# Kernel tuning notes

Hardware: AMD Instinct MI355X
Metric: run time of the kernel (lower is better)

## Reference

```python
import jax, jax.numpy as jnp
jax.config.update("jax_enable_x64", True)  # morton codes need int64 bit tricks
import numpy as np

B = 8
N_POINTS = 131072
PATCH = 32
STRIDE = 16
RES = 1024
D_MODEL = 256
L = (N_POINTS - PATCH) // STRIDE + 1  # 8191


def setup_inputs() -> dict:
    key = jax.random.key(0)
    ks = jax.random.split(key, 11)
    def lin_w(k, fin, fout):
        return (jax.random.normal(k, (fin, fout), jnp.float32) / np.sqrt(fin)).astype(jnp.float32)
    return {
        "points": jax.random.normal(ks[0], (B, N_POINTS, 3), jnp.float32),
        # LocalGeometryEncoder mlp: 3 -> 64 -> 128 (ReLU after both)
        "W1": lin_w(ks[1], 3, 64), "b1": jnp.zeros((64,), jnp.float32),
        "W2": lin_w(ks[2], 64, 128), "b2": jnp.zeros((128,), jnp.float32),
        # PositionalEncoding mlp: 3 -> 64 -> 128 (ReLU only after first)
        "Wp1": lin_w(ks[3], 3, 64), "bp1": jnp.zeros((64,), jnp.float32),
        "Wp2": lin_w(ks[4], 64, 128), "bp2": jnp.zeros((128,), jnp.float32),
        # projection: 256 -> d_model
        "Wproj": lin_w(ks[5], 256, D_MODEL), "bproj": jnp.zeros((D_MODEL,), jnp.float32),
    }


def _expand_bits(v):
    v = v.astype(jnp.int64)
    v = (v | (v << 32)) & jnp.int64(8725724278095871)
    v = (v | (v << 16)) & jnp.int64(8725728556220671)
    v = (v | (v << 8)) & jnp.int64(1157144660301377551)
    v = (v | (v << 4)) & jnp.int64(1207822528635744451)
    v = (v | (v << 2)) & jnp.int64(1317624576693539401)
    return v


def _morton_code(points):
    p_min = points.min(axis=1, keepdims=True)
    p_max = points.max(axis=1, keepdims=True)
    scale = jnp.clip(p_max - p_min, 1e-8, None)
    normed = (points - p_min) / scale
    q = jnp.clip((normed * (RES - 1)).astype(jnp.int64), 0, RES - 1)  # [B,N,3]
    return _expand_bits(q[..., 0]) * 4 + _expand_bits(q[..., 1]) * 2 + _expand_bits(q[..., 2])


def reference(points, W1, b1, W2, b2, Wp1, bp1, Wp2, bp2, Wproj, bproj):
    # z-order sort
    morton = _morton_code(points)                 # [B,N] int64
    sort_idx = jnp.argsort(morton, axis=1)        # [B,N]
    sp = jnp.take_along_axis(points, sort_idx[..., None], axis=1)  # [B,N,3]
    # sliding-window unfold -> [B,L,P,3]
    win = jnp.arange(L)[:, None] * STRIDE + jnp.arange(PATCH)[None, :]  # [L,P]
    patches = sp[:, win, :]
    # local geometry encoder
    centroids = patches.mean(axis=2)              # [B,L,3]
    local = patches - centroids[:, :, None, :]    # [B,L,P,3]
    h = jax.nn.relu(jnp.einsum('blpc,cd->blpd', local, W1) + b1)
    feat = jax.nn.relu(jnp.einsum('blpd,de->blpe', h, W2) + b2)  # [B,L,P,128]
    geo = feat.max(axis=2)                        # [B,L,128]
    # positional encoding of centroids
    pos = jax.nn.relu(centroids @ Wp1 + bp1) @ Wp2 + bp2  # [B,L,128]
    combined = jnp.concatenate([geo, pos], axis=-1)       # [B,L,256]
    tokens = combined @ Wproj + bproj                     # [B,L,d_model]
    return tokens, centroids, sort_idx
```

## Files before the change

kernel.cpp:

```cpp
#include <hip/hip_runtime.h>
#include <hip/hip_bf16.h>
#include <stdint.h>

#define B_SZ   8
#define N_PTS  131072
#define L_TOK  8191
#define M_TOK  (B_SZ * L_TOK)

typedef unsigned long long u64;
typedef unsigned int u32;
typedef unsigned short u16;
typedef __hip_bfloat16 bf16;
typedef float f32x4 __attribute__((ext_vector_type(4)));
typedef short bf16x8 __attribute__((ext_vector_type(8)));
typedef u32 u32x4 __attribute__((ext_vector_type(4)));

__device__ __forceinline__ u16 f2bf(float f) {
  u32 u = __float_as_uint(f);
  u32 r = u + 0x7FFFu + ((u >> 16) & 1u);
  return (u16)(r >> 16);
}
__device__ __forceinline__ float bf2f(u16 s) {
  return __uint_as_float(((u32)s) << 16);
}

__device__ __forceinline__ void split_pair(float h0, float h1, u32& hp, u32& lp) {
  asm("v_cvt_pk_bf16_f32 %0, %1, %2" : "=v"(hp) : "v"(h0), "v"(h1));
  float r0 = __uint_as_float(hp << 16);
  float r1 = __uint_as_float(hp & 0xFFFF0000u);
  asm("v_cvt_pk_bf16_f32 %0, %1, %2" : "=v"(lp) : "v"(h0 - r0), "v"(h1 - r1));
}
__device__ __forceinline__ bf16x8 asbf(u32x4 x) {
  union { u32x4 a; bf16x8 b; } u; u.a = x; return u.b;
}

__device__ __forceinline__ u32 f2u_mono(float f) {
  u32 u = __float_as_uint(f);
  return (u & 0x80000000u) ? ~u : (u | 0x80000000u);
}
__device__ __forceinline__ float u2f_mono(u32 u) {
  u32 b = (u & 0x80000000u) ? (u ^ 0x80000000u) : ~u;
  return __uint_as_float(b);
}

__global__ void init_mm_kernel(u32* mm) {
  int t = threadIdx.x;
  if (t < 48) mm[t] = ((t % 6) < 3) ? 0xFFFFFFFFu : 0u;
}

__global__ __launch_bounds__(256) void minmax_kernel(const float* __restrict__ pts,
                                                     u32* __restrict__ mm) {
  int b = blockIdx.x >> 6;
  int chunk = blockIdx.x & 63;
  int base = b * N_PTS + chunk * 2048;
  float mn0 = 3.4e38f, mn1 = 3.4e38f, mn2 = 3.4e38f;
  float mx0 = -3.4e38f, mx1 = -3.4e38f, mx2 = -3.4e38f;
  for (int i = threadIdx.x; i < 2048; i += 256) {
    const float* p = pts + (size_t)(base + i) * 3;
    float x = p[0], y = p[1], z = p[2];
    mn0 = fminf(mn0, x); mx0 = fmaxf(mx0, x);
    mn1 = fminf(mn1, y); mx1 = fmaxf(mx1, y);
    mn2 = fminf(mn2, z); mx2 = fmaxf(mx2, z);
  }
  __shared__ u32 smn[3], smx[3];
  if (threadIdx.x < 3) { smn[threadIdx.x] = 0xFFFFFFFFu; smx[threadIdx.x] = 0u; }
  __syncthreads();
  atomicMin(&smn[0], f2u_mono(mn0)); atomicMin(&smn[1], f2u_mono(mn1)); atomicMin(&smn[2], f2u_mono(mn2));
  atomicMax(&smx[0], f2u_mono(mx0)); atomicMax(&smx[1], f2u_mono(mx1)); atomicMax(&smx[2], f2u_mono(mx2));
  __syncthreads();
  if (threadIdx.x < 3)       atomicMin(&mm[b * 6 + threadIdx.x], smn[threadIdx.x]);
  else if (threadIdx.x < 6)  atomicMax(&mm[b * 6 + threadIdx.x], smx[threadIdx.x - 3]);
}

__device__ __forceinline__ u64 expand_bits(u64 v) {
  v = (v | (v << 32)) & 0x001F00000000FFFFull;
  v = (v | (v << 16)) & 0x001F0000FF0000FFull;
  v = (v | (v << 8))  & 0x100F00F00F00F00Full;
  v = (v | (v << 4))  & 0x10C30C30C30C30C3ull;
  v = (v | (v << 2))  & 0x1249249249249249ull;
  return v;
}

__device__ __forceinline__ long long quant1(float p, float mn, float mx) {
  float scale = fmaxf(mx - mn, 1e-8f);
  float num = p - mn;
  float rcp = 1.0f / scale;
  asm volatile("" : "+v"(rcp));
  float normed = num * rcp;
  asm volatile("" : "+v"(normed));
  float scaled = normed * 1023.0f;
  asm volatile("" : "+v"(scaled));
  long long q = (long long)scaled;
  q = q < 0 ? 0 : q; q = q > 1023 ? 1023 : q;
  return q;
}

__global__ __launch_bounds__(256) void morton_kernel(const float* __restrict__ pts,
                                                     const u32* __restrict__ mm,
                                                     u64* __restrict__ keys) {
  int gid = blockIdx.x * 256 + threadIdx.x;
  int b = gid >> 17;
  int i = gid & (N_PTS - 1);
  const u32* mb = mm + b * 6;
  float mn0 = u2f_mono(mb[0]), mn1 = u2f_mono(mb[1]), mn2 = u2f_mono(mb[2]);
  float mx0 = u2f_mono(mb[3]), mx1 = u2f_mono(mb[4]), mx2 = u2f_mono(mb[5]);
  const float* p = pts + (size_t)gid * 3;
  long long q0 = quant1(p[0], mn0, mx0);
  long long q1 = quant1(p[1], mn1, mx1);
  long long q2 = quant1(p[2], mn2, mx2);
  u64 m = expand_bits((u64)q0) * 4ull + expand_bits((u64)q1) * 2ull + expand_bits((u64)q2);
  keys[gid] = (m << 17) | (u64)i;
}

__global__ __launch_bounds__(256) void radix_hist(const u64* __restrict__ keys,
                                                  u32* __restrict__ hist, int shift) {
  int blk = blockIdx.x;
  int b = blk >> 8, c = blk & 255;
  int t = threadIdx.x;
  __shared__ u32 h[256];
  h[t] = 0;
  __syncthreads();
  size_t base = ((size_t)b << 17) + (size_t)c * 512;
  u32 d0 = (u32)((keys[base + t] >> shift) & 255ull);
  u32 d1 = (u32)((keys[base + 256 + t] >> shift) & 255ull);
  atomicAdd(&h[d0], 1u);
  atomicAdd(&h[d1], 1u);
  __syncthreads();
  hist[(blk << 8) + t] = h[t];
}

__global__ __launch_bounds__(256) void radix_scan_a(u32* __restrict__ hist,
                                                    u32* __restrict__ tot) {
  int blk = blockIdx.x;
  int b = blk >> 3, dg = blk & 7;
  int t = threadIdx.x;
  __shared__ u32 H[32 * 257];
  __shared__ u32 part[32 * 8];
  for (int i = t; i < 8192; i += 256) {
    int c = i >> 5, d5 = i & 31;
    H[d5 * 257 + c] = hist[((b * 256 + c) << 8) + dg * 32 + d5];
  }
  __syncthreads();
  int d5 = t & 31, sub = t >> 5;
  u32 s = 0;
  for (int c = sub * 32; c < sub * 32 + 32; ++c) s += H[d5 * 257 + c];
  part[d5 * 8 + sub] = s;
  __syncthreads();
  u32 run = 0;
  for (int k = 0; k < sub; ++k) run += part[d5 * 8 + k];
  if (sub == 7) tot[(b << 8) + dg * 32 + d5] = run + s;
  for (int c = sub * 32; c < sub * 32 + 32; ++c) {
    u32 x = H[d5 * 257 + c];
    H[d5 * 257 + c] = run;
    run += x;
  }
  __syncthreads();
  for (int i = t; i < 8192; i += 256) {
    int c = i >> 5, d5b = i & 31;
    hist[((b * 256 + c) << 8) + dg * 32 + d5b] = H[d5b * 257 + c];
  }
}

__global__ __launch_bounds__(256) void radix_scan_b(const u32* __restrict__ tot,
                                                    u32* __restrict__ dbase) {
  int b = blockIdx.x;
  int t = threadIdx.x;
  __shared__ u32 s[256];
  u32 my = tot[(b << 8) + t];
  s[t] = my;
  __syncthreads();
  for (int off = 1; off < 256; off <<= 1) {
    u32 v = (t >= off) ? s[t - off] : 0u;
    __syncthreads();
    s[t] += v;
    __syncthreads();
  }
  dbase[(b << 8) + t] = s[t] - my;
}

__global__ __launch_bounds__(512) void radix_scatter(const u64* __restrict__ keys_in,
                                                     u64* __restrict__ keys_out,
                                                     const u32* __restrict__ hist,
                                                     const u32* __restrict__ dbase,
                                                     int shift) {
  int blk = blockIdx.x;
  int b = blk >> 8, c = blk & 255;
  int t = threadIdx.x;
  int w = t >> 6, lane = t & 63;
  __shared__ u32 whist[8][256];
  __shared__ u32 gbase[256];
  for (int i = t; i < 2048; i += 512) ((u32*)whist)[i] = 0u;
  if (t < 256) gbase[t] = hist[(blk << 8) + t] + dbase[(b << 8) + t];
  __syncthreads();
  size_t base = ((size_t)b << 17) + (size_t)c * 512;
  u64 key = keys_in[base + t];
  u32 d = (u32)((key >> shift) & 255ull);
  u64 m = ~0ull;
  #pragma unroll
  for (int k = 0; k < 8; ++k) {
    u64 bb = __ballot((d >> k) & 1u);
    m &= ((d >> k) & 1u) ? bb : ~bb;
  }
  u32 rank = (u32)__popcll(m & ((1ull << lane) - 1ull));
  int leader = (int)(__ffsll((unsigned long long)m)) - 1;
  if (lane == (u32)leader) whist[w][d] = (u32)__popcll(m);
  __syncthreads();
  if (t < 256) {
    u32 run = 0;
    #pragma unroll
    for (int ww = 0; ww < 8; ++ww) { u32 v = whist[ww][t]; whist[ww][t] = run; run += v; }
  }
  __syncthreads();
  u32 dst = gbase[d] + whist[w][d] + rank;
  keys_out[((size_t)b << 17) + dst] = key;
}

__global__ __launch_bounds__(256) void extract_frag_kernel(
    const u64* __restrict__ keys, const float* __restrict__ pts,
    float* __restrict__ sp, float* __restrict__ sidx,
    const float* __restrict__ Wproj, const float* __restrict__ W2,
    const float* __restrict__ Wp2,
    u16* __restrict__ wfrag, u16* __restrict__ w2f, u16* __restrict__ wp2f) {
  int bid = blockIdx.x;
  int t = threadIdx.x;
  if (bid < 4096) {
    int gid = bid * 256 + t;
    u64 key = keys[gid];
    int idx = (int)(key & 0x1FFFFull);
    sidx[gid] = (float)idx;
    int b = gid >> 17;
    const float* src = pts + ((size_t)(b << 17) + idx) * 3;
    float* dst = sp + (size_t)gid * 3;
    dst[0] = src[0]; dst[1] = src[1]; dst[2] = src[2];
  } else {
    int fb = bid - 4096;
    if (fb < 256) {
      int e = fb * 256 + t;
      int k = e >> 8, n = e & 255;
      float v = Wproj[e];
      u16 hb = f2bf(v);
      u16 lb = f2bf(v - bf2f(hb));
      int ks = k >> 5, q = (k >> 3) & 3, j = k & 7;
      int nt = n >> 4, ln2 = n & 15;
      int base = ((ks * 16 + nt) * 64 + q * 16 + ln2) * 8 + j;
      wfrag[base] = hb;
      wfrag[65536 + base] = lb;
    } else {
      const float* W = (fb < 288) ? W2 : Wp2;
      u16* frag = (fb < 288) ? w2f : wp2f;
      int e = ((fb < 288) ? (fb - 256) : (fb - 288)) * 256 + t;
      int k = e >> 7, n = e & 127;
      float v = W[e];
      u16 hb = f2bf(v);
      u16 lb = f2bf(v - bf2f(hb));
      int kc = k >> 5, q = (k >> 3) & 3, j = k & 7;
      int nt = n >> 4, ln2 = n & 15;
      int base = ((kc * 8 + nt) * 64 + q * 16 + ln2) * 8 + j;
      frag[base] = hb;
      frag[8192 + base] = lb;
    }
  }
}

__global__ __launch_bounds__(512) void patch_kernel(
    const float* __restrict__ sp,
    const float* __restrict__ W1, const float* __restrict__ b1,
    const u16* __restrict__ W2g, const float* __restrict__ b2,
    const float* __restrict__ Wp1, const float* __restrict__ bp1,
    const u16* __restrict__ Wp2g, const float* __restrict__ bp2,
    bf16* __restrict__ comb, float* __restrict__ cent_out) {
  __shared__ float ptsS[6192];
  __shared__ float cenS[384];
  __shared__ float w1p[256];
  __shared__ float wpp[256];
  __shared__ float b2s[128];
  __shared__ float bp2s[128];
  __shared__ __align__(16) u16 W2frag[16384];

  int t = threadIdx.x;
  int bib = blockIdx.x;
  int b = blockIdx.y;
  int l0 = bib * 128;
  int pcount = min(128, L_TOK - l0);

  {
    const float4* src4 = (const float4*)(sp + (size_t)b * (N_PTS * 3) + (size_t)l0 * 48);
    int nvec = min(1548, ((N_PTS - l0 * 16) * 3) >> 2);
    float4* dst4 = (float4*)ptsS;
    for (int i = t; i < nvec; i += 512) dst4[i] = src4[i];
  }
  {
    const float4* s4 = (const float4*)W2g;
    float4* d4 = (float4*)W2frag;
    for (int i = t; i < 2048; i += 512) d4[i] = s4[i];
  }
  if (t < 64) {
    w1p[t] = W1[t]; w1p[64 + t] = W1[64 + t];
    w1p[128 + t] = W1[128 + t]; w1p[192 + t] = b1[t];
  } else if (t < 128) {
    int i = t - 64;
    wpp[i] = Wp1[i]; wpp[64 + i] = Wp1[64 + i];
    wpp[128 + i] = Wp1[128 + i]; wpp[192 + i] = bp1[i];
  } else if (t < 256) {
    b2s[t - 128] = b2[t - 128];
  } else if (t < 384) {
    bp2s[t - 256] = bp2[t - 256];
  }
  __syncthreads();

  if (t < 384) {
    int pa = t / 3, c = t - pa * 3;
    if (pa < pcount) {
      float s = 0.f;
      for (int i = 0; i < 32; ++i) {
        int ii = (i + pa) & 31;
        s += ptsS[(pa * 16 + ii) * 3 + c];
      }
      float cv = s * (1.0f / 32.0f);
      cenS[pa * 3 + c] = cv;
      cent_out[(size_t)(b * L_TOK + l0 + pa) * 3 + c] = cv;
    }
  }
  __syncthreads();

  int w = t >> 6, lane = t & 63, ln = lane & 15, quad = lane >> 4;
  const bf16x8* Bf = (const bf16x8*)W2frag;

  for (int ig = 0; ig < 16; ++ig) {
    int ll = w * 16 + ig;
    if (ll >= pcount) break;
    float cx = cenS[ll * 3], cy = cenS[ll * 3 + 1], cz = cenS[ll * 3 + 2];
    float xs[2], ys[2], zs[2];
    #pragma unroll
    for (int mt = 0; mt < 2; ++mt) {
      int row = ll * 16 + mt * 16 + ln;
      xs[mt] = ptsS[row * 3] - cx;
      ys[mt] = ptsS[row * 3 + 1] - cy;
      zs[mt] = ptsS[row * 3 + 2] - cz;
    }
    u32x4 Ahi[2][2], Alo[2][2];
    #pragma unroll
    for (int kc = 0; kc < 2; ++kc)
      #pragma unroll
      for (int w4 = 0; w4 < 4; ++w4) {
        int col = kc * 32 + quad * 8 + w4 * 2;
        float wx0 = w1p[col],     wy0 = w1p[64 + col],     wz0 = w1p[128 + col],     wb0 = w1p[192 + col];
        float wx1 = w1p[col + 1], wy1 = w1p[64 + col + 1], wz1 = w1p[128 + col + 1], wb1 = w1p[192 + col + 1];
        #pragma unroll
        for (int mt = 0; mt < 2; ++mt) {
          float h0 = fmaxf(fmaf(xs[mt], wx0, fmaf(ys[mt], wy0, fmaf(zs[mt], wz0, wb0))), 0.f);
          float h1 = fmaxf(fmaf(xs[mt], wx1, fmaf(ys[mt], wy1, fmaf(zs[mt], wz1, wb1))), 0.f);
          u32 hp, lp;
          split_pair(h0, h1, hp, lp);
          Ahi[mt][kc][w4] = hp;
          Alo[mt][kc][w4] = lp;
        }
      }
    bf16x8 Ah[2][2], Al[2][2];
    #pragma unroll
    for (int mt = 0; mt < 2; ++mt)
      #pragma unroll
      for (int kc = 0; kc < 2; ++kc) { Ah[mt][kc] = asbf(Ahi[mt][kc]); Al[mt][kc] = asbf(Alo[mt][kc]); }

    size_t tokoff = (size_t)(b * L_TOK + l0 + ll) * 256;
    #pragma unroll
    for (int half = 0; half < 2; ++half) {
      f32x4 acc[2][4];
      #pragma unroll
      for (int mt = 0; mt < 2; ++mt)
        #pragma unroll
        for (int n4 = 0; n4 < 4; ++n4) acc[mt][n4] = (f32x4){0.f, 0.f, 0.f, 0.f};
      #pragma unroll
      for (int n4 = 0; n4 < 4; ++n4) {
        int nt = half * 4 + n4;
        bf16x8 Bh0 = Bf[(0 * 8 + nt) * 64 + lane];
        bf16x8 Bh1 = Bf[(1 * 8 + nt) * 64 + lane];
        bf16x8 Bl0 = Bf[1024 + (0 * 8 + nt) * 64 + lane];
        bf16x8 Bl1 = Bf[1024 + (1 * 8 + nt) * 64 + lane];
        #pragma unroll
        for (int mt = 0; mt < 2; ++mt) {
          acc[mt][n4] = __builtin_amdgcn_mfma_f32_16x16x32_bf16(Ah[mt][0], Bh0, acc[mt][n4], 0, 0, 0);
          acc[mt][n4] = __builtin_amdgcn_mfma_f32_16x16x32_bf16(Ah[mt][1], Bh1, acc[mt][n4], 0, 0, 0);
          acc[mt][n4] = __builtin_amdgcn_mfma_f32_16x16x32_bf16(Al[mt][0], Bh0, acc[mt][n4], 0, 0, 0);
          acc[mt][n4] = __builtin_amdgcn_mfma_f32_16x16x32_bf16(Al[mt][1], Bh1, acc[mt][n4], 0, 0, 0);
          acc[mt][n4] = __builtin_amdgcn_mfma_f32_16x16x32_bf16(Ah[mt][0], Bl0, acc[mt][n4], 0, 0, 0);
          acc[mt][n4] = __builtin_amdgcn_mfma_f32_16x16x32_bf16(Ah[mt][1], Bl1, acc[mt][n4], 0, 0, 0);
        }
      }
      #pragma unroll
      for (int n4 = 0; n4 < 4; ++n4) {
        int col = (half * 4 + n4) * 16 + ln;
        float bv = b2s[col];
        float m = 0.f;
        #pragma unroll
        for (int mt = 0; mt < 2; ++mt)
          #pragma unroll
          for (int r = 0; r < 4; ++r) m = fmaxf(m, acc[mt][n4][r] + bv);
        m = fmaxf(m, __shfl_xor(m, 16));
        m = fmaxf(m, __shfl_xor(m, 32));
        if (lane < 16) comb[tokoff + col] = __float2bfloat16(m);
      }
    }
  }

  {
    int lrow = w * 16 + ln;
    int lcl = min(lrow, pcount - 1);
    float cx = cenS[lcl * 3], cy = cenS[lcl * 3 + 1], cz = cenS[lcl * 3 + 2];
    u32x4 Ahi[2], Alo[2];
    #pragma unroll
    for (int kc = 0; kc < 2; ++kc)
      #pragma unroll
      for (int w4 = 0; w4 < 4; ++w4) {
        int col = kc * 32 + quad * 8 + w4 * 2;
        float h0 = fmaxf(fmaf(cx, wpp[col], fmaf(cy, wpp[64 + col], fmaf(cz, wpp[128 + col], wpp[192 + col]))), 0.f);
        float h1 = fmaxf(fmaf(cx, wpp[col + 1], fmaf(cy, wpp[64 + col + 1], fmaf(cz, wpp[128 + col + 1], wpp[192 + col + 1]))), 0.f);
        u32 hp, lp;
        split_pair(h0, h1, hp, lp);
        Ahi[kc][w4] = hp;
        Alo[kc][w4] = lp;
      }
    bf16x8 A0h = asbf(Ahi[0]), A1h = asbf(Ahi[1]), A0l = asbf(Alo[0]), A1l = asbf(Alo[1]);
    const bf16x8* Pf = (const bf16x8*)Wp2g;
    f32x4 acc[8];
    #pragma unroll
    for (int nt = 0; nt < 8; ++nt) acc[nt] = (f32x4){0.f, 0.f, 0.f, 0.f};
    #pragma unroll
    for (int nt = 0; nt < 8; ++nt) {
      bf16x8 Bh0 = Pf[(0 * 8 + nt) * 64 + lane];
      bf16x8 Bh1 = Pf[(8 + nt) * 64 + lane];
      bf16x8 Bl0 = Pf[1024 + (0 * 8 + nt) * 64 + lane];
      bf16x8 Bl1 = Pf[1024 + (8 + nt) * 64 + lane];
      acc[nt] = __builtin_amdgcn_mfma_f32_16x16x32_bf16(A0h, Bh0, acc[nt], 0, 0, 0);
      acc[nt] = __builtin_amdgcn_mfma_f32_16x16x32_bf16(A1h, Bh1, acc[nt], 0, 0, 0);
      acc[nt] = __builtin_amdgcn_mfma_f32_16x16x32_bf16(A0l, Bh0, acc[nt], 0, 0, 0);
      acc[nt] = __builtin_amdgcn_mfma_f32_16x16x32_bf16(A1l, Bh1, acc[nt], 0, 0, 0);
      acc[nt] = __builtin_amdgcn_mfma_f32_16x16x32_bf16(A0h, Bl0, acc[nt], 0, 0, 0);
      acc[nt] = __builtin_amdgcn_mfma_f32_16x16x32_bf16(A1h, Bl1, acc[nt], 0, 0, 0);
    }
    #pragma unroll
    for (int nt = 0; nt < 8; ++nt)
      #pragma unroll
      for (int r = 0; r < 4; ++r) {
        int lr = w * 16 + quad * 4 + r;
        if (lr < pcount) {
          float v = acc[nt][r] + bp2s[nt * 16 + ln];
          comb[(size_t)(b * L_TOK + l0 + lr) * 256 + 128 + nt * 16 + ln] = __float2bfloat16(v);
        }
      }
  }
}

__global__ __launch_bounds__(256) void proj_mfma(const bf16* __restrict__ A,
                                                 const u16* __restrict__ fragG,
                                                 const float* __restrict__ bias,
                                                 float* __restrict__ C) {
  int t = threadIdx.x;
  int w = t >> 6, lane = t & 63, ln = lane & 15, quad = lane >> 4;
  int tile0 = blockIdx.x * 8 + w * 2;
  const bf16x8* Bf = (const bf16x8*)fragG;

  bf16x8 Af[2][8];
  const bf16x8 zero8 = (bf16x8){0, 0, 0, 0, 0, 0, 0, 0};
  #pragma unroll
  for (int mt = 0; mt < 2; ++mt) {
    int row = (tile0 + mt) * 16 + ln;
    bool ok = row < M_TOK;
    const bf16x8* ap = (const bf16x8*)(A + (size_t)(ok ? row : 0) * 256);
    #pragma unroll
    for (int ks = 0; ks < 8; ++ks) {
      bf16x8 v = ap[ks * 4 + quad];
      Af[mt][ks] = ok ? v : zero8;
    }
  }

  for (int nt = 0; nt < 16; ++nt) {
    f32x4 acc[2];
    #pragma unroll
    for (int mt = 0; mt < 2; ++mt) acc[mt] = (f32x4){0.f, 0.f, 0.f, 0.f};
    #pragma unroll
    for (int ks = 0; ks < 8; ++ks) {
      bf16x8 Bh = Bf[(ks * 16 + nt) * 64 + lane];
      bf16x8 Bl = Bf[8192 + (ks * 16 + nt) * 64 + lane];
      #pragma unroll
      for (int mt = 0; mt < 2; ++mt)
        acc[mt] = __builtin_amdgcn_mfma_f32_16x16x32_bf16(Af[mt][ks], Bh, acc[mt], 0, 0, 0);
      #pragma unroll
      for (int mt = 0; mt < 2; ++mt)
        acc[mt] = __builtin_amdgcn_mfma_f32_16x16x32_bf16(Af[mt][ks], Bl, acc[mt], 0, 0, 0);
    }
    int col = nt * 16 + ln;
    float bv = bias[col];
    #pragma unroll
    for (int mt = 0; mt < 2; ++mt)
      #pragma unroll
      for (int r = 0; r < 4; ++r) {
        int row = (tile0 + mt) * 16 + quad * 4 + r;
        if (row < M_TOK) C[(size_t)row * 256 + col] = acc[mt][r] + bv;
      }
  }
}

extern "C" void kernel_launch(void* const* d_in, const int* in_sizes, int n_in,
                              void* d_out, int out_size, void* d_ws, size_t ws_size,
                              hipStream_t stream) {
  const float* points = (const float*)d_in[0];
  const float* W1 = (const float*)d_in[1];
  const float* b1 = (const float*)d_in[2];
  const float* W2 = (const float*)d_in[3];
  const float* b2 = (const float*)d_in[4];
  const float* Wp1 = (const float*)d_in[5];
  const float* bp1 = (const float*)d_in[6];
  const float* Wp2 = (const float*)d_in[7];
  const float* bp2 = (const float*)d_in[8];
  const float* Wproj = (const float*)d_in[9];
  const float* bproj = (const float*)d_in[10];

  float* out = (float*)d_out;
  float* tokens = out;
  float* cents  = out + 16775168;
  float* sidx   = out + 16971752;

  char* ws = (char*)d_ws;
  u32* mm     = (u32*)ws;
  u64* keysA  = (u64*)(ws + 256);
  float* sp   = (float*)(ws + 256 + 8388608);
  char* combB = ws + 256 + 8388608 + 12582912;
  bf16* comb  = (bf16*)combB;
  u64* keysB  = (u64*)combB;
  u32* hist   = (u32*)(combB + 8388608);
  u32* totG   = (u32*)(combB + 8388608 + 2097152);
  u32* dbase  = (u32*)(combB + 8388608 + 2097152 + 8192);
  u16* wfrag  = (u16*)(ws + 256);
  u16* w2fg   = (u16*)(ws + 256 + 262144);
  u16* wp2fg  = (u16*)(ws + 256 + 262144 + 32768);

  init_mm_kernel<<<1, 64, 0, stream>>>(mm);
  minmax_kernel<<<512, 256, 0, stream>>>(points, mm);
  morton_kernel<<<4096, 256, 0, stream>>>(points, mm, keysA);

  const int shifts[4] = {17, 25, 33, 41};
  u64* src = keysA; u64* dst = keysB;
  for (int p = 0; p < 4; ++p) {
    radix_hist<<<2048, 256, 0, stream>>>(src, hist, shifts[p]);
    radix_scan_a<<<64, 256, 0, stream>>>(hist, totG);
    radix_scan_b<<<8, 256, 0, stream>>>(totG, dbase);
    radix_scatter<<<2048, 512, 0, stream>>>(src, dst, hist, dbase, shifts[p]);
    u64* tmp = src; src = dst; dst = tmp;
  }

  extract_frag_kernel<<<4416, 256, 0, stream>>>(src, points, sp, sidx,
                                                Wproj, W2, Wp2, wfrag, w2fg, wp2fg);
  patch_kernel<<<dim3(64, 8), 512, 0, stream>>>(sp, W1, b1, w2fg, b2,
                                                Wp1, bp1, wp2fg, bp2, comb, cents);
  proj_mfma<<<512, 256, 0, stream>>>(comb, wfrag, bproj, tokens);
}
```

Measured before the change: 370.2 us.

## Process 2048 keys per radix block and widen proj_mfma row tiles

Each radix histogram/scatter block now handles 2048 keys instead of 512, so there are 64 chunks per batch instead of 256. The scan kernel shrinks accordingly and the histogram buffer it reads and writes is smaller. The scatter ranks four keys per wave using warp-level match plus shared atomics, keeping the sort stable because keys are wave-contiguous. proj_mfma now gives each wave 4 M-tiles and splits the N dimension across two blocks, so each B fragment load feeds more MFMAs at the cost of more registers.

```diff
diff --git a/kernel.cpp b/kernel.cpp
--- a/kernel.cpp
+++ b/kernel.cpp
@@ -112,21 +112,22 @@
   keys[gid] = (m << 17) | (u64)i;
 }
 
-__global__ __launch_bounds__(256) void radix_hist(const u64* __restrict__ keys,
+__global__ __launch_bounds__(512) void radix_hist(const u64* __restrict__ keys,
                                                   u32* __restrict__ hist, int shift) {
   int blk = blockIdx.x;
-  int b = blk >> 8, c = blk & 255;
+  int b = blk >> 6, c = blk & 63;
   int t = threadIdx.x;
   __shared__ u32 h[256];
-  h[t] = 0;
-  __syncthreads();
-  size_t base = ((size_t)b << 17) + (size_t)c * 512;
-  u32 d0 = (u32)((keys[base + t] >> shift) & 255ull);
-  u32 d1 = (u32)((keys[base + 256 + t] >> shift) & 255ull);
-  atomicAdd(&h[d0], 1u);
-  atomicAdd(&h[d1], 1u);
-  __syncthreads();
-  hist[(blk << 8) + t] = h[t];
+  if (t < 256) h[t] = 0;
+  __syncthreads();
+  size_t base = ((size_t)b << 17) + (size_t)c * 2048;
+  #pragma unroll
+  for (int i = 0; i < 4; ++i) {
+    u32 d = (u32)((keys[base + i * 512 + t] >> shift) & 255u);
+    atomicAdd(&h[d], 1u);
+  }
+  __syncthreads();
+  if (t < 256) hist[(blk << 8) + t] = h[t];
 }
 
 __global__ __launch_bounds__(256) void radix_scan_a(u32* __restrict__ hist,
@@ -134,30 +135,30 @@
   int blk = blockIdx.x;
   int b = blk >> 3, dg = blk & 7;
   int t = threadIdx.x;
-  __shared__ u32 H[32 * 257];
+  __shared__ u32 H[32 * 65];
   __shared__ u32 part[32 * 8];
-  for (int i = t; i < 8192; i += 256) {
+  for (int i = t; i < 2048; i += 256) {
     int c = i >> 5, d5 = i & 31;
-    H[d5 * 257 + c] = hist[((b * 256 + c) << 8) + dg * 32 + d5];
+    H[d5 * 65 + c] = hist[((b * 64 + c) << 8) + dg * 32 + d5];
   }
   __syncthreads();
   int d5 = t & 31, sub = t >> 5;
   u32 s = 0;
-  for (int c = sub * 32; c < sub * 32 + 32; ++c) s += H[d5 * 257 + c];
+  for (int c = sub * 8; c < sub * 8 + 8; ++c) s += H[d5 * 65 + c];
   part[d5 * 8 + sub] = s;
   __syncthreads();
   u32 run = 0;
   for (int k = 0; k < sub; ++k) run += part[d5 * 8 + k];
   if (sub == 7) tot[(b << 8) + dg * 32 + d5] = run + s;
-  for (int c = sub * 32; c < sub * 32 + 32; ++c) {
-    u32 x = H[d5 * 257 + c];
-    H[d5 * 257 + c] = run;
+  for (int c = sub * 8; c < sub * 8 + 8; ++c) {
+    u32 x = H[d5 * 65 + c];
+    H[d5 * 65 + c] = run;
     run += x;
   }
   __syncthreads();
-  for (int i = t; i < 8192; i += 256) {
+  for (int i = t; i < 2048; i += 256) {
     int c = i >> 5, d5b = i & 31;
-    hist[((b * 256 + c) << 8) + dg * 32 + d5b] = H[d5b * 257 + c];
+    hist[((b * 64 + c) << 8) + dg * 32 + d5b] = H[d5b * 65 + c];
   }
 }
 
@@ -184,7 +185,7 @@
                                                      const u32* __restrict__ dbase,
                                                      int shift) {
   int blk = blockIdx.x;
-  int b = blk >> 8, c = blk & 255;
+  int b = blk >> 6, c = blk & 63;
   int t = threadIdx.x;
   int w = t >> 6, lane = t & 63;
   __shared__ u32 whist[8][256];
@@ -192,18 +193,29 @@
   for (int i = t; i < 2048; i += 512) ((u32*)whist)[i] = 0u;
   if (t < 256) gbase[t] = hist[(blk << 8) + t] + dbase[(b << 8) + t];
   __syncthreads();
-  size_t base = ((size_t)b << 17) + (size_t)c * 512;
-  u64 key = keys_in[base + t];
-  u32 d = (u32)((key >> shift) & 255ull);
-  u64 m = ~0ull;
+  size_t base = ((size_t)b << 17) + (size_t)c * 2048;
+  u64 key[4]; u32 dig[4]; u32 loff[4];
   #pragma unroll
-  for (int k = 0; k < 8; ++k) {
-    u64 bb = __ballot((d >> k) & 1u);
-    m &= ((d >> k) & 1u) ? bb : ~bb;
-  }
-  u32 rank = (u32)__popcll(m & ((1ull << lane) - 1ull));
-  int leader = (int)(__ffsll((unsigned long long)m)) - 1;
-  if (lane == (u32)leader) whist[w][d] = (u32)__popcll(m);
+  for (int i = 0; i < 4; ++i) {
+    key[i] = keys_in[base + w * 256 + i * 64 + lane];
+    dig[i] = (u32)((key[i] >> shift) & 255u);
+  }
+  #pragma unroll
+  for (int i = 0; i < 4; ++i) {
+    u64 m = ~0ull;
+    #pragma unroll
+    for (int k = 0; k < 8; ++k) {
+      u64 bb = __ballot((dig[i] >> k) & 1u);
+      m &= ((dig[i] >> k) & 1u) ? bb : ~bb;
+    }
+    u32 rank = (u32)__popcll(m & ((1ull << lane) - 1ull));
+    u32 cnt = (u32)__popcll(m);
+    int leader = (int)__ffsll((unsigned long long)m) - 1;
+    u32 prev = 0;
+    if (lane == leader) prev = atomicAdd(&whist[w][dig[i]], cnt);
+    prev = __shfl(prev, leader);
+    loff[i] = prev + rank;
+  }
   __syncthreads();
   if (t < 256) {
     u32 run = 0;
@@ -211,8 +223,11 @@
     for (int ww = 0; ww < 8; ++ww) { u32 v = whist[ww][t]; whist[ww][t] = run; run += v; }
   }
   __syncthreads();
-  u32 dst = gbase[d] + whist[w][d] + rank;
-  keys_out[((size_t)b << 17) + dst] = key;
+  #pragma unroll
+  for (int i = 0; i < 4; ++i) {
+    u32 dst = gbase[dig[i]] + whist[w][dig[i]] + loff[i];
+    keys_out[((size_t)b << 17) + dst] = key[i];
+  }
 }
 
 __global__ __launch_bounds__(256) void extract_frag_kernel(
@@ -457,13 +472,15 @@
                                                  float* __restrict__ C) {
   int t = threadIdx.x;
   int w = t >> 6, lane = t & 63, ln = lane & 15, quad = lane >> 4;
-  int tile0 = blockIdx.x * 8 + w * 2;
+  int mg = blockIdx.x >> 1;
+  int nh = blockIdx.x & 1;
+  int tile0 = mg * 16 + w * 4;
   const bf16x8* Bf = (const bf16x8*)fragG;
 
-  bf16x8 Af[2][8];
+  bf16x8 Af[4][8];
   const bf16x8 zero8 = (bf16x8){0, 0, 0, 0, 0, 0, 0, 0};
   #pragma unroll
-  for (int mt = 0; mt < 2; ++mt) {
+  for (int mt = 0; mt < 4; ++mt) {
     int row = (tile0 + mt) * 16 + ln;
     bool ok = row < M_TOK;
     const bf16x8* ap = (const bf16x8*)(A + (size_t)(ok ? row : 0) * 256);
@@ -474,25 +491,26 @@
     }
   }
 
-  for (int nt = 0; nt < 16; ++nt) {
-    f32x4 acc[2];
-    #pragma unroll
-    for (int mt = 0; mt < 2; ++mt) acc[mt] = (f32x4){0.f, 0.f, 0.f, 0.f};
+  for (int nt2 = 0; nt2 < 8; ++nt2) {
+    int nt = nh * 8 + nt2;
+    f32x4 acc[4];
+    #pragma unroll
+    for (int mt = 0; mt < 4; ++mt) acc[mt] = (f32x4){0.f, 0.f, 0.f, 0.f};
     #pragma unroll
     for (int ks = 0; ks < 8; ++ks) {
       bf16x8 Bh = Bf[(ks * 16 + nt) * 64 + lane];
       bf16x8 Bl = Bf[8192 + (ks * 16 + nt) * 64 + lane];
       #pragma unroll
-      for (int mt = 0; mt < 2; ++mt)
+      for (int mt = 0; mt < 4; ++mt)
         acc[mt] = __builtin_amdgcn_mfma_f32_16x16x32_bf16(Af[mt][ks], Bh, acc[mt], 0, 0, 0);
       #pragma unroll
-      for (int mt = 0; mt < 2; ++mt)
+      for (int mt = 0; mt < 4; ++mt)
         acc[mt] = __builtin_amdgcn_mfma_f32_16x16x32_bf16(Af[mt][ks], Bl, acc[mt], 0, 0, 0);
     }
     int col = nt * 16 + ln;
     float bv = bias[col];
     #pragma unroll
-    for (int mt = 0; mt < 2; ++mt)
+    for (int mt = 0; mt < 4; ++mt)
       #pragma unroll
       for (int r = 0; r < 4; ++r) {
         int row = (tile0 + mt) * 16 + quad * 4 + r;
@@ -542,10 +560,10 @@
   const int shifts[4] = {17, 25, 33, 41};
   u64* src = keysA; u64* dst = keysB;
   for (int p = 0; p < 4; ++p) {
-    radix_hist<<<2048, 256, 0, stream>>>(src, hist, shifts[p]);
+    radix_hist<<<512, 512, 0, stream>>>(src, hist, shifts[p]);
     radix_scan_a<<<64, 256, 0, stream>>>(hist, totG);
     radix_scan_b<<<8, 256, 0, stream>>>(totG, dbase);
-    radix_scatter<<<2048, 512, 0, stream>>>(src, dst, hist, dbase, shifts[p]);
+    radix_scatter<<<512, 512, 0, stream>>>(src, dst, hist, dbase, shifts[p]);
     u64* tmp = src; src = dst; dst = tmp;
   }
 
```

New measurement: 352.1 us. 1.05x faster.
